# Performance work log

Measured on AMD Instinct MI355X. Metric: run time of the kernel, lower is better.

Reference implementation:

```python
import jax, jax.numpy as jnp
import numpy as np

B, S, D = 32, 128, 1024      # encoder batch, seq len, embed_dim
C = 65536                    # nclasses (sense inventory)
N = 512                      # number of gathered WSD target tokens
NNZ = 262144                 # nnz of sparse label adjacency A (avg degree 4)
EPS = 1e-5                   # BatchNorm1d eps


def setup_inputs() -> dict:
    key = jax.random.key(0)
    ks = jax.random.split(key, 7)
    enc_out = jax.random.normal(ks[0], (B, S, D), dtype=jnp.float32)
    batch_idx = jax.random.randint(ks[1], (N,), 0, B)
    tgt = jax.random.randint(ks[2], (N,), 0, S)
    A_indices = jax.random.randint(ks[3], (2, NNZ), 0, C)
    A_values = jax.random.uniform(ks[4], (NNZ,), dtype=jnp.float32)
    wt2_w = jax.random.normal(ks[5], (C, D), dtype=jnp.float32) / np.sqrt(D).astype(np.float32)
    wt2_b = jax.random.normal(ks[6], (C,), dtype=jnp.float32) * 0.02
    return {"enc_out": enc_out, "wt2_w": wt2_w, "wt2_b": wt2_b,
            "A_values": A_values, "batch_idx": batch_idx, "tgt": tgt,
            "A_indices": A_indices}


def reference(enc_out, wt2_w, wt2_b, A_values, batch_idx, tgt, A_indices):
    # gather target-token embeddings: [N, D]
    g = enc_out[batch_idx, tgt]
    # BatchNorm1d(affine=False), training mode -> batch stats, biased var
    mean = jnp.mean(g, axis=0)
    var = jnp.var(g, axis=0)
    h0 = (g - mean) / jnp.sqrt(var + EPS)
    # wt2 Linear + swish -> logits over classes Z: [N, C]
    h1 = jax.nn.swish(h0 @ wt2_w.T + wt2_b)
    # sparse spmm: torch_sparse.spmm(ii, vv, m=C, n=C, matrix=Z.T).T == Z @ A.T
    row, col = A_indices[0], A_indices[1]
    gathered = h1.T[col] * A_values[:, None]            # [NNZ, N]
    neighbors = jax.ops.segment_sum(gathered, row, num_segments=C).T  # [N, C]
    # residual add (renormalize=False)
    return neighbors + h1
```

## Files before the change

### kernel.cpp

```cpp
#include <hip/hip_runtime.h>
#include <hip/hip_bf16.h>

typedef unsigned short u16;
typedef unsigned int   u32;
typedef __attribute__((ext_vector_type(8))) short bf16x8;
typedef __attribute__((ext_vector_type(4))) float f32x4;

static constexpr int kS = 128, kD = 1024, kC = 65536, kN = 512, kNNZ = 262144;

__device__ __forceinline__ u16 f2bf(float x) {
  u32 u = __float_as_uint(x);
  u32 r = (u + 0x7fffu + ((u >> 16) & 1u)) >> 16;
  return (u16)r;
}
__device__ __forceinline__ u32 pack2(float a, float b) {
  return (u32)f2bf(a) | ((u32)f2bf(b) << 16);
}
__device__ __forceinline__ u32 pk(float a, float b) {
  __hip_bfloat162 h = __float22bfloat162_rn(float2{a, b});
  union { __hip_bfloat162 v; u32 u; } c; c.v = h;
  return c.u;
}
__device__ __forceinline__ float bf_lo(u32 v) { return __uint_as_float(v << 16); }
__device__ __forceinline__ float bf_hi(u32 v) { return __uint_as_float(v & 0xffff0000u); }

__device__ __forceinline__ void gload16(const void* g, void* l) {
  __builtin_amdgcn_global_load_lds(
      (const __attribute__((address_space(1))) void*)g,
      (__attribute__((address_space(3))) void*)l, 16, 0, 0);
}

__global__ void k_bn_part(const float* __restrict__ enc, const int* __restrict__ bidx,
                          const int* __restrict__ tgt, float* __restrict__ part) {
  __shared__ int offs[64];
  int n0 = blockIdx.y * 64;
  if (threadIdx.x < 64) offs[threadIdx.x] = bidx[n0 + threadIdx.x] * kS + tgt[n0 + threadIdx.x];
  __syncthreads();
  int d = blockIdx.x * 256 + threadIdx.x;
  float s = 0.f, ss = 0.f;
  for (int i = 0; i < 64; ++i) {
    float v = enc[(size_t)offs[i] * kD + d];
    s += v; ss += v * v;
  }
  part[(blockIdx.y * 2 + 0) * kD + d] = s;
  part[(blockIdx.y * 2 + 1) * kD + d] = ss;
}

__global__ void k_bn_fin(const float* __restrict__ part, float* __restrict__ mean,
                         float* __restrict__ rstd) {
  int d = blockIdx.x * 256 + threadIdx.x;
  float s = 0.f, ss = 0.f;
#pragma unroll
  for (int b = 0; b < 8; ++b) {
    s  += part[(b * 2 + 0) * kD + d];
    ss += part[(b * 2 + 1) * kD + d];
  }
  float m = s * (1.f / kN);
  float var = ss * (1.f / kN) - m * m;
  mean[d] = m;
  rstd[d] = 1.f / sqrtf(var + 1e-5f);
}

__global__ void k_bn_pack(const float* __restrict__ enc, const int* __restrict__ bidx,
                          const int* __restrict__ tgt, const float* __restrict__ mean,
                          const float* __restrict__ rstd, u16* __restrict__ Bp) {
  int i = blockIdx.x * 256 + threadIdx.x;
  int n = i & 511;
  int g = i >> 9;
  int k0 = g * 8;
  size_t src = (size_t)(bidx[n] * kS + tgt[n]) * kD + k0;
  float4 v0 = *(const float4*)(enc + src);
  float4 v1 = *(const float4*)(enc + src + 4);
  float4 m0 = *(const float4*)(mean + k0);
  float4 m1 = *(const float4*)(mean + k0 + 4);
  float4 r0 = *(const float4*)(rstd + k0);
  float4 r1 = *(const float4*)(rstd + k0 + 4);
  u32 q0 = pack2((v0.x - m0.x) * r0.x, (v0.y - m0.y) * r0.y);
  u32 q1 = pack2((v0.z - m0.z) * r0.z, (v0.w - m0.w) * r0.w);
  u32 q2 = pack2((v1.x - m1.x) * r1.x, (v1.y - m1.y) * r1.y);
  u32 q3 = pack2((v1.z - m1.z) * r1.z, (v1.w - m1.w) * r1.w);
  *(uint4*)(Bp + (size_t)i * 8) = make_uint4(q0, q1, q2, q3);
}

__global__ void k_hist(const int* __restrict__ rows, int* __restrict__ hist) {
  int e = blockIdx.x * blockDim.x + threadIdx.x;
  if (e < kNNZ) atomicAdd(&hist[rows[e]], 1);
}

__global__ __launch_bounds__(1024) void k_scan(int* __restrict__ hist, int* __restrict__ cursor) {
  __shared__ int sm[1024];
  int t = threadIdx.x;
  int base = t * 64;
  int sum = 0;
  for (int i = 0; i < 64; ++i) sum += hist[base + i];
  sm[t] = sum;
  __syncthreads();
  for (int off = 1; off < 1024; off <<= 1) {
    int v = (t >= off) ? sm[t - off] : 0;
    __syncthreads();
    sm[t] += v;
    __syncthreads();
  }
  int run = sm[t] - sum;
  for (int i = 0; i < 64; ++i) {
    int v = hist[base + i];
    hist[base + i] = run;
    cursor[base + i] = run;
    run += v;
  }
  if (t == 1023) hist[kC] = run;
}

__global__ void k_scatter(const int* __restrict__ rows, const int* __restrict__ cols,
                          const float* __restrict__ vals, int* __restrict__ cursor,
                          int* __restrict__ scol, float* __restrict__ sval) {
  int e = blockIdx.x * blockDim.x + threadIdx.x;
  if (e < kNNZ) {
    int r = rows[e];
    int p = atomicAdd(&cursor[r], 1);
    scol[p] = cols[e];
    sval[p] = vals[e];
  }
}

__global__ __launch_bounds__(1024, 4)
void k_gemm_f7(const float* __restrict__ W, const u16* __restrict__ Bp,
               const float* __restrict__ bias, u16* __restrict__ h1t) {
  __shared__ __align__(16) u16 Bb[2][16384];
  __shared__ __align__(16) u16 Ab[2][4096];
  const int t = threadIdx.x;
  const int l = t & 63, w = t >> 6;
  const int wm = w >> 3, wn = (w & 7) * 64;
  const int cb = blockIdx.x * 128;
  const int q = l >> 4, ln = l & 15;

  const u16* gB0 = Bp + (size_t)t * 8;
  const u16* gB1 = Bp + (size_t)(t + 1024) * 8;

  const int sr = t >> 2;
  const float* gA = W + (size_t)(cb + sr) * kD + (t & 3) * 8;
  const int aws = sr * 32 + (((t & 3) ^ (sr & 3)) * 8);

  f32x4 acc[4][4];
#pragma unroll
  for (int a = 0; a < 4; ++a)
#pragma unroll
    for (int b = 0; b < 4; ++b) acc[a][b] = (f32x4){0.f, 0.f, 0.f, 0.f};

  gload16(gB0, (char*)Bb[0] + t * 16);
  gload16(gB1, (char*)Bb[0] + (t + 1024) * 16);
  if (t < 512) {
    float4 a0 = *(const float4*)(gA);
    float4 a1 = *(const float4*)(gA + 4);
    *(uint4*)(&Ab[0][aws]) =
        make_uint4(pk(a0.x, a0.y), pk(a0.z, a0.w), pk(a1.x, a1.y), pk(a1.z, a1.w));
  }
  __syncthreads();

#pragma unroll 2
  for (int tt = 0; tt < 32; ++tt) {
    const int cur = tt & 1;
    float4 na0, na1;
    if (tt < 31) {
      gload16(gB0 + (size_t)(tt + 1) * 16384, (char*)Bb[cur ^ 1] + t * 16);
      gload16(gB1 + (size_t)(tt + 1) * 16384, (char*)Bb[cur ^ 1] + (t + 1024) * 16);
      if (t < 512) {
        na0 = *(const float4*)(gA + (tt + 1) * 32);
        na1 = *(const float4*)(gA + (tt + 1) * 32 + 4);
      }
    }
    bf16x8 bv[4], af[4];
#pragma unroll
    for (int nb = 0; nb < 4; ++nb)
      bv[nb] = *(const bf16x8*)(&Bb[cur][(q * 512 + wn + nb * 16 + ln) * 8]);
#pragma unroll
    for (int mb = 0; mb < 4; ++mb) {
      int rr = wm * 64 + mb * 16 + ln;
      af[mb] = *(const bf16x8*)(&Ab[cur][rr * 32 + ((q ^ (rr & 3)) * 8)]);
    }
#pragma unroll
    for (int mb = 0; mb < 4; ++mb)
#pragma unroll
      for (int nb = 0; nb < 4; ++nb)
        acc[mb][nb] = __builtin_amdgcn_mfma_f32_16x16x32_bf16(af[mb], bv[nb], acc[mb][nb], 0, 0, 0);
    if (tt < 31 && t < 512) {
      *(uint4*)(&Ab[cur ^ 1][aws]) =
          make_uint4(pk(na0.x, na0.y), pk(na0.z, na0.w), pk(na1.x, na1.y), pk(na1.z, na1.w));
    }
    __syncthreads();
  }

#pragma unroll
  for (int mb = 0; mb < 4; ++mb) {
    int rb = wm * 64 + mb * 16 + q * 4;
#pragma unroll
    for (int i = 0; i < 4; ++i) {
      int c = cb + rb + i;
      float bvs = bias[c];
#pragma unroll
      for (int nb = 0; nb < 4; ++nb) {
        float x = acc[mb][nb][i] + bvs;
        float sw = x / (1.f + __expf(-x));
        h1t[(size_t)c * kN + (wn + nb * 16 + ln)] = f2bf(sw);
      }
    }
  }
}

#define FMA8(cv, v)                                                        \
  a0 = fmaf(v, bf_lo(cv.x), a0); a1 = fmaf(v, bf_hi(cv.x), a1);            \
  a2 = fmaf(v, bf_lo(cv.y), a2); a3 = fmaf(v, bf_hi(cv.y), a3);            \
  a4 = fmaf(v, bf_lo(cv.z), a4); a5 = fmaf(v, bf_hi(cv.z), a5);            \
  a6 = fmaf(v, bf_lo(cv.w), a6); a7 = fmaf(v, bf_hi(cv.w), a7);

__global__ __launch_bounds__(512)
void k_spmm(const u16* __restrict__ h1t, const int* __restrict__ rowptr,
            const int* __restrict__ scol, const float* __restrict__ sval,
            float* __restrict__ out) {
  __shared__ float tile[32 * 512];
  int r0 = blockIdx.x * 32;
  int t = threadIdx.x, w = t >> 6, l = t & 63;
#pragma unroll
  for (int j = 0; j < 4; ++j) {
    int rl = w * 4 + j;
    int r = r0 + rl;
    uint4 hv = ((const uint4*)(h1t + (size_t)r * kN))[l];
    float a0 = bf_lo(hv.x), a1 = bf_hi(hv.x), a2 = bf_lo(hv.y), a3 = bf_hi(hv.y);
    float a4 = bf_lo(hv.z), a5 = bf_hi(hv.z), a6 = bf_lo(hv.w), a7 = bf_hi(hv.w);
    int e0 = rowptr[r], e1 = rowptr[r + 1];
    uint4 cv0 = {}, cv1 = {};
    float v0 = 0.f, v1 = 0.f;
    if (e0 < e1) {
      v0 = sval[e0];
      cv0 = ((const uint4*)(h1t + (size_t)scol[e0] * kN))[l];
    }
    if (e0 + 1 < e1) {
      v1 = sval[e0 + 1];
      cv1 = ((const uint4*)(h1t + (size_t)scol[e0 + 1] * kN))[l];
    }
    for (int e = e0; e < e1; e += 2) {
      FMA8(cv0, v0);
      if (e + 2 < e1) {
        v0 = sval[e + 2];
        cv0 = ((const uint4*)(h1t + (size_t)scol[e + 2] * kN))[l];
      }
      if (e + 1 < e1) {
        FMA8(cv1, v1);
        if (e + 3 < e1) {
          v1 = sval[e + 3];
          cv1 = ((const uint4*)(h1t + (size_t)scol[e + 3] * kN))[l];
        }
      }
    }
    int sw = (rl & 7) << 2;
    *(float4*)&tile[rl * 512 + ((8 * l) ^ sw)]     = make_float4(a0, a1, a2, a3);
    *(float4*)&tile[rl * 512 + ((8 * l + 4) ^ sw)] = make_float4(a4, a5, a6, a7);
  }
  __syncthreads();
  int r = l & 31;
  int swr = (r & 7) << 2;
#pragma unroll
  for (int it = 0; it < 32; ++it) {
    int n = it * 16 + w * 2 + (l >> 5);
    out[(size_t)n * kC + r0 + r] = tile[r * 512 + (n ^ swr)];
  }
}

extern "C" void kernel_launch(void* const* d_in, const int* in_sizes, int n_in,
                              void* d_out, int out_size, void* d_ws, size_t ws_size,
                              hipStream_t stream) {
  (void)in_sizes; (void)n_in; (void)out_size; (void)ws_size;
  const float* enc   = (const float*)d_in[0];
  const float* W     = (const float*)d_in[1];
  const float* bias  = (const float*)d_in[2];
  const float* Avals = (const float*)d_in[3];
  const int*   bidx  = (const int*)d_in[4];
  const int*   tgt   = (const int*)d_in[5];
  const int*   Arow  = (const int*)d_in[6];
  const int*   Acol  = Arow + kNNZ;
  float* out = (float*)d_out;

  char* ws = (char*)d_ws;
  float* mean   = (float*)(ws);
  float* rstd   = (float*)(ws + 4096);
  u16*   Bp     = (u16*)  (ws + 8192);
  int*   rowptr = (int*)  (ws + 1056768);
  int*   cursor = (int*)  (ws + 1319168);
  int*   scol   = (int*)  (ws + 1581312);
  float* sval   = (float*)(ws + 2629888);
  float* part   = (float*)(ws + 3678464);
  u16*   h1t    = (u16*)  (ws + 4194304);

  hipMemsetAsync(rowptr, 0, (kC + 1) * sizeof(int), stream);
  k_bn_part<<<dim3(4, 8), 256, 0, stream>>>(enc, bidx, tgt, part);
  k_bn_fin<<<4, 256, 0, stream>>>(part, mean, rstd);
  k_bn_pack<<<256, 256, 0, stream>>>(enc, bidx, tgt, mean, rstd, Bp);
  k_hist<<<kNNZ / 256, 256, 0, stream>>>(Arow, rowptr);
  k_scan<<<1, 1024, 0, stream>>>(rowptr, cursor);
  k_scatter<<<kNNZ / 256, 256, 0, stream>>>(Arow, Acol, Avals, cursor, scol, sval);
  k_gemm_f7<<<512, 1024, 0, stream>>>(W, Bp, bias, h1t);
  k_spmm<<<kC / 32, 512, 0, stream>>>(h1t, rowptr, scol, sval, out);
}
```

Measured before the change: 293.1 us.

## Double K-step per barrier in GEMM with larger LDS stages and MFMA priority

The fused GEMM+swish kernel now processes two 32-wide K slices per barrier iteration, using 160KB of LDS for double-buffered 64-wide K stages. All 1024 threads now share the W fp32-to-bf16 conversion instead of half of them. The second A-slice global load is deferred until between the two MFMA groups, and s_setprio is raised around the MFMA blocks. The aim is to halve the number of __syncthreads and overlap loads better. In exchange, launch bounds drop to one block per CU and the larger LDS footprint reduces occupancy.

```diff
diff --git a/kernel.cpp b/kernel.cpp
--- a/kernel.cpp
+++ b/kernel.cpp
@@ -123,23 +123,21 @@
   }
 }
 
-__global__ __launch_bounds__(1024, 4)
-void k_gemm_f7(const float* __restrict__ W, const u16* __restrict__ Bp,
+__global__ __launch_bounds__(1024, 1)
+void k_gemm_f8(const float* __restrict__ W, const u16* __restrict__ Bp,
                const float* __restrict__ bias, u16* __restrict__ h1t) {
-  __shared__ __align__(16) u16 Bb[2][16384];
-  __shared__ __align__(16) u16 Ab[2][4096];
+  __shared__ __align__(16) u16 lds[81920];
+  u16* Bb = lds;
+  u16* Ab = lds + 65536;
   const int t = threadIdx.x;
   const int l = t & 63, w = t >> 6;
   const int wm = w >> 3, wn = (w & 7) * 64;
   const int cb = blockIdx.x * 128;
   const int q = l >> 4, ln = l & 15;
 
-  const u16* gB0 = Bp + (size_t)t * 8;
-  const u16* gB1 = Bp + (size_t)(t + 1024) * 8;
-
-  const int sr = t >> 2;
-  const float* gA = W + (size_t)(cb + sr) * kD + (t & 3) * 8;
-  const int aws = sr * 32 + (((t & 3) ^ (sr & 3)) * 8);
+  const int ar = t >> 3, as = t & 7;
+  const float* gA = W + (size_t)(cb + ar) * kD + as * 4;
+  const int awoff = ar * 32 + (((as >> 1) ^ (ar & 3)) * 8) + (as & 1) * 4;
 
   f32x4 acc[4][4];
 #pragma unroll
@@ -147,45 +145,81 @@
 #pragma unroll
     for (int b = 0; b < 4; ++b) acc[a][b] = (f32x4){0.f, 0.f, 0.f, 0.f};
 
-  gload16(gB0, (char*)Bb[0] + t * 16);
-  gload16(gB1, (char*)Bb[0] + (t + 1024) * 16);
-  if (t < 512) {
+  {
     float4 a0 = *(const float4*)(gA);
-    float4 a1 = *(const float4*)(gA + 4);
-    *(uint4*)(&Ab[0][aws]) =
-        make_uint4(pk(a0.x, a0.y), pk(a0.z, a0.w), pk(a1.x, a1.y), pk(a1.z, a1.w));
+    float4 a1 = *(const float4*)(gA + 32);
+    gload16(Bp + (size_t)t * 8,               (char*)Bb + t * 16);
+    gload16(Bp + (size_t)(t + 1024) * 8,      (char*)Bb + (t + 1024) * 16);
+    gload16(Bp + (size_t)(2048 + t) * 8,      (char*)Bb + 32768 + t * 16);
+    gload16(Bp + (size_t)(2048 + t + 1024) * 8, (char*)Bb + 32768 + (t + 1024) * 16);
+    *(uint2*)(Ab + awoff)        = make_uint2(pk(a0.x, a0.y), pk(a0.z, a0.w));
+    *(uint2*)(Ab + 4096 + awoff) = make_uint2(pk(a1.x, a1.y), pk(a1.z, a1.w));
   }
   __syncthreads();
 
 #pragma unroll 2
-  for (int tt = 0; tt < 32; ++tt) {
-    const int cur = tt & 1;
-    float4 na0, na1;
-    if (tt < 31) {
-      gload16(gB0 + (size_t)(tt + 1) * 16384, (char*)Bb[cur ^ 1] + t * 16);
-      gload16(gB1 + (size_t)(tt + 1) * 16384, (char*)Bb[cur ^ 1] + (t + 1024) * 16);
-      if (t < 512) {
-        na0 = *(const float4*)(gA + (tt + 1) * 32);
-        na1 = *(const float4*)(gA + (tt + 1) * 32 + 4);
-      }
-    }
-    bf16x8 bv[4], af[4];
-#pragma unroll
-    for (int nb = 0; nb < 4; ++nb)
-      bv[nb] = *(const bf16x8*)(&Bb[cur][(q * 512 + wn + nb * 16 + ln) * 8]);
-#pragma unroll
-    for (int mb = 0; mb < 4; ++mb) {
-      int rr = wm * 64 + mb * 16 + ln;
-      af[mb] = *(const bf16x8*)(&Ab[cur][rr * 32 + ((q ^ (rr & 3)) * 8)]);
-    }
-#pragma unroll
-    for (int mb = 0; mb < 4; ++mb)
+  for (int ss = 0; ss < 16; ++ss) {
+    const int cu = ss & 1, nx = cu ^ 1;
+    const u16* Bc = Bb + cu * 32768 / 2;
+    const u16* Ac = Ab + cu * 8192 / 2;
+    const u16* Bc0 = Bb + cu * 32768;
+    const u16* Bc1 = Bc0 + 16384;
+    const u16* Ac0 = Ab + cu * 8192;
+    const u16* Ac1 = Ac0 + 4096;
+    (void)Bc; (void)Ac;
+
+    float4 nA0, nA1;
+    if (ss < 15) {
+      const int ph = (ss + 1) * 2;
+      nA0 = *(const float4*)(gA + ph * 32);
+      char* Bn = (char*)(Bb + nx * 32768);
+      gload16(Bp + ((size_t)ph * 2048 + t) * 8,              Bn + t * 16);
+      gload16(Bp + ((size_t)ph * 2048 + t + 1024) * 8,       Bn + (t + 1024) * 16);
+      gload16(Bp + ((size_t)(ph + 1) * 2048 + t) * 8,        Bn + 32768 + t * 16);
+      gload16(Bp + ((size_t)(ph + 1) * 2048 + t + 1024) * 8, Bn + 32768 + (t + 1024) * 16);
+    }
+    __builtin_amdgcn_s_setprio(1);
+    {
+      bf16x8 bv[4], af[4];
 #pragma unroll
       for (int nb = 0; nb < 4; ++nb)
-        acc[mb][nb] = __builtin_amdgcn_mfma_f32_16x16x32_bf16(af[mb], bv[nb], acc[mb][nb], 0, 0, 0);
-    if (tt < 31 && t < 512) {
-      *(uint4*)(&Ab[cur ^ 1][aws]) =
-          make_uint4(pk(na0.x, na0.y), pk(na0.z, na0.w), pk(na1.x, na1.y), pk(na1.z, na1.w));
+        bv[nb] = *(const bf16x8*)(Bc0 + (q * 512 + wn + nb * 16 + ln) * 8);
+#pragma unroll
+      for (int mb = 0; mb < 4; ++mb) {
+        int rr = wm * 64 + mb * 16 + ln;
+        af[mb] = *(const bf16x8*)(Ac0 + rr * 32 + ((q ^ (rr & 3)) * 8));
+      }
+#pragma unroll
+      for (int mb = 0; mb < 4; ++mb)
+#pragma unroll
+        for (int nb = 0; nb < 4; ++nb)
+          acc[mb][nb] = __builtin_amdgcn_mfma_f32_16x16x32_bf16(af[mb], bv[nb], acc[mb][nb], 0, 0, 0);
+    }
+    __builtin_amdgcn_s_setprio(0);
+    if (ss < 15) {
+      *(uint2*)(Ab + nx * 8192 + awoff) = make_uint2(pk(nA0.x, nA0.y), pk(nA0.z, nA0.w));
+      nA1 = *(const float4*)(gA + ((ss + 1) * 2 + 1) * 32);
+    }
+    __builtin_amdgcn_s_setprio(1);
+    {
+      bf16x8 bv[4], af[4];
+#pragma unroll
+      for (int nb = 0; nb < 4; ++nb)
+        bv[nb] = *(const bf16x8*)(Bc1 + (q * 512 + wn + nb * 16 + ln) * 8);
+#pragma unroll
+      for (int mb = 0; mb < 4; ++mb) {
+        int rr = wm * 64 + mb * 16 + ln;
+        af[mb] = *(const bf16x8*)(Ac1 + rr * 32 + ((q ^ (rr & 3)) * 8));
+      }
+#pragma unroll
+      for (int mb = 0; mb < 4; ++mb)
+#pragma unroll
+        for (int nb = 0; nb < 4; ++nb)
+          acc[mb][nb] = __builtin_amdgcn_mfma_f32_16x16x32_bf16(af[mb], bv[nb], acc[mb][nb], 0, 0, 0);
+    }
+    __builtin_amdgcn_s_setprio(0);
+    if (ss < 15) {
+      *(uint2*)(Ab + nx * 8192 + 4096 + awoff) = make_uint2(pk(nA1.x, nA1.y), pk(nA1.z, nA1.w));
     }
     __syncthreads();
   }
@@ -298,6 +332,6 @@
   k_hist<<<kNNZ / 256, 256, 0, stream>>>(Arow, rowptr);
   k_scan<<<1, 1024, 0, stream>>>(rowptr, cursor);
   k_scatter<<<kNNZ / 256, 256, 0, stream>>>(Arow, Acol, Avals, cursor, scol, sval);
-  k_gemm_f7<<<512, 1024, 0, stream>>>(W, Bp, bias, h1t);
+  k_gemm_f8<<<kC / 128, 1024, 0, stream>>>(W, Bp, bias, h1t);
   k_spmm<<<kC / 32, 512, 0, stream>>>(h1t, rowptr, scol, sval, out);
 }
```

After: 321.5 us. 1.1x slower.
